# Kernel tuning notes

Measured on AMD Instinct MI355X. Metric: run time of the kernel, lower is better.

Reference implementation:

```python
import jax, jax.numpy as jnp
import numpy as np
import math

N_HEAD = 4
NORM_GROUPS = 32
EPS = 1e-5


def setup_inputs() -> dict:
    key = jax.random.key(0)
    ks = jax.random.split(key, 6)
    C = 256
    x = jax.random.normal(ks[0], (2, C, 64, 64), dtype=jnp.float32)
    gn_w = jnp.ones((C,), dtype=jnp.float32)
    gn_b = jnp.zeros((C,), dtype=jnp.float32)
    s = 1.0 / math.sqrt(C)
    wq = jax.random.normal(ks[1], (C, C), dtype=jnp.float32) * s
    wk = jax.random.normal(ks[2], (C, C), dtype=jnp.float32) * s
    wv = jax.random.normal(ks[3], (C, C), dtype=jnp.float32) * s
    wo = jax.random.normal(ks[4], (C, C), dtype=jnp.float32) * s
    bo = jnp.zeros((C,), dtype=jnp.float32)
    return {"x": x, "gn_w": gn_w, "gn_b": gn_b, "wq": wq, "wk": wk,
            "wv": wv, "wo": wo, "bo": bo}


def group_norm(x, w, b):
    bsz, c, h, wd = x.shape
    xg = x.reshape(bsz, NORM_GROUPS, c // NORM_GROUPS, h, wd)
    mu = jnp.mean(xg, axis=(2, 3, 4), keepdims=True)
    var = jnp.mean(jnp.square(xg - mu), axis=(2, 3, 4), keepdims=True)
    xn = ((xg - mu) * jax.lax.rsqrt(var + EPS)).reshape(bsz, c, h, wd)
    return xn * w[None, :, None, None] + b[None, :, None, None]


def conv1x1(x, w):
    # w: (out_ch, in_ch) applied pointwise
    return jnp.einsum('bchw,oc->bohw', x, w)


def reference(x, gn_w, gn_b, wq, wk, wv, wo, bo):
    bsz, c, h, w = x.shape
    hd = c // N_HEAD
    norm = group_norm(x, gn_w, gn_b)
    q = conv1x1(norm, wq).reshape(bsz, N_HEAD, hd, h, w)
    k = conv1x1(norm, wk).reshape(bsz, N_HEAD, hd, h, w)
    v = conv1x1(norm, wv).reshape(bsz, N_HEAD, hd, h, w)
    # scores over full spatial positions; NOTE: scaled by sqrt(channel), as in source
    scores = jnp.einsum('bnchw,bncxy->bnhwxy', q, k) / jnp.sqrt(jnp.float32(c))
    probs = jax.nn.softmax(scores.reshape(bsz, N_HEAD, h, w, h * w), axis=-1)
    probs = probs.reshape(bsz, N_HEAD, h, w, h, w)
    out = jnp.einsum('bnhwxy,bncxy->bnchw', probs, v).reshape(bsz, c, h, w)
    out = conv1x1(out, wo) + bo[None, :, None, None]
    return out + x
```

## Files before the change

### kernel.cpp

```cpp
#include <hip/hip_runtime.h>

typedef float f32x4 __attribute__((ext_vector_type(4)));
typedef float f32x16 __attribute__((ext_vector_type(16)));
typedef short bf16x8 __attribute__((ext_vector_type(8)));
typedef unsigned short u16;
typedef unsigned int u32;
typedef unsigned int u32x2 __attribute__((ext_vector_type(2)));

#define MFMA(a, b, c) __builtin_amdgcn_mfma_f32_16x16x32_bf16((a), (b), (c), 0, 0, 0)
#define MFMA32(a, b, c) __builtin_amdgcn_mfma_f32_32x32x16_bf16((a), (b), (c), 0, 0, 0)

static __device__ __forceinline__ u16 f2bf(float f) {
    union { float f; u32 u; } v; v.f = f;
    u32 r = v.u + 0x7FFFu + ((v.u >> 16) & 1u);
    return (u16)(r >> 16);
}

static __device__ __forceinline__ u32 pkbf(float a, float b) {
    u32 ua = __float_as_uint(a) + 0x8000u;
    u32 ub = __float_as_uint(b) + 0x8000u;
    return __builtin_amdgcn_perm(ub, ua, 0x07060302);
}

static __device__ __forceinline__ void gll16(const u16* g, u16* l) {
    __builtin_amdgcn_global_load_lds(
        (const __attribute__((address_space(1))) u32*)(const void*)g,
        (__attribute__((address_space(3))) u32*)(void*)l, 16, 0, 0);
}

#define BAR_VM() do { \
    asm volatile("s_waitcnt vmcnt(0)" ::: "memory"); \
    __builtin_amdgcn_s_barrier(); \
    asm volatile("" ::: "memory"); \
} while (0)

#define BAR_LGKM() do { \
    asm volatile("s_waitcnt lgkmcnt(0)" ::: "memory"); \
    __builtin_amdgcn_s_barrier(); \
} while (0)

__global__ __launch_bounds__(256) void prep_kernel(
    const float* __restrict__ wq, const float* __restrict__ wk,
    const float* __restrict__ wv, const float* __restrict__ wo,
    const float* __restrict__ x, u16* __restrict__ Wbf,
    float2* __restrict__ part) {
    int blk = blockIdx.x;
    int t = threadIdx.x;
    if (blk < 256) {
        int base = (blk * 256 + t) * 4;
        int p = base >> 16;
        int off = base & 65535;
        const float* W = (p == 0) ? wq : ((p == 1) ? wk : ((p == 2) ? wv : wo));
        float sc = (p == 0) ? 0.09014009048f : 1.0f;
        float4 v = *(const float4*)(W + off);
        uint2 pk;
        pk.x = pkbf(v.x * sc, v.y * sc);
        pk.y = pkbf(v.z * sc, v.w * sc);
        *(uint2*)(Wbf + base) = pk;
        return;
    }
    int sblk = blk - 256;
    int bg = sblk >> 2, quarter = sblk & 3;
    const float* xp = x + (size_t)bg * 32768 + quarter * 8192;

    float s = 0.f, ss = 0.f;
#pragma unroll
    for (int rep = 0; rep < 8; ++rep) {
        float4 v = *(const float4*)(xp + t * 4 + rep * 1024);
        s += v.x + v.y + v.z + v.w;
        ss += v.x * v.x + v.y * v.y + v.z * v.z + v.w * v.w;
    }
    for (int off = 1; off < 64; off <<= 1) {
        s += __shfl_xor(s, off);
        ss += __shfl_xor(ss, off);
    }
    __shared__ float red[8];
    int lane = t & 63, w = t >> 6;
    if (lane == 0) { red[w] = s; red[4 + w] = ss; }
    __syncthreads();
    if (t == 0) {
        part[sblk] = make_float2(red[0] + red[1] + red[2] + red[3],
                                 red[4] + red[5] + red[6] + red[7]);
    }
}

__global__ __launch_bounds__(256) void qkv_gemm(
    const float* __restrict__ x, const float* __restrict__ gw,
    const float* __restrict__ gb, const float2* __restrict__ part,
    const u16* __restrict__ Wbf,
    u16* __restrict__ Q, u16* __restrict__ K, u16* __restrict__ V) {
    int b = blockIdx.y & 1;
    int p = blockIdx.y >> 1;
    const u16* W = Wbf + p * 65536;
    int bx = blockIdx.x;
    int m0 = ((bx >> 3) & 1) * 128;
    int n0 = ((bx & 7) | ((bx >> 4) << 3)) * 64;

    __shared__ u16 a_s[2][128 * 40];
    __shared__ u16 b_s[2][64 * 40];
    __shared__ float wgt_s[256], bia_s[256];

    int t = threadIdx.x;
    int lane = t & 63, wave = t >> 6;
    int wm = wave & 1, wn = wave >> 1;
    int r = lane & 15, qd = lane >> 4;

    {
        int c = t;
        int g = c >> 3;
        float s = 0.f, ss = 0.f;
#pragma unroll
        for (int q = 0; q < 4; ++q) {
            float2 pp = part[(b * 32 + g) * 4 + q];
            s += pp.x; ss += pp.y;
        }
        float mu = s * (1.f / 32768.f);
        float var = ss * (1.f / 32768.f) - mu * mu;
        float rstd = rsqrtf(var + 1e-5f);
        float wg = gw[c] * rstd;
        wgt_s[c] = wg;
        bia_s[c] = gb[c] - mu * wg;
    }
    __syncthreads();

    f32x4 acc[4][2];
#pragma unroll
    for (int i = 0; i < 4; ++i)
#pragma unroll
        for (int j = 0; j < 2; ++j) acc[i][j] = (f32x4){0.f, 0.f, 0.f, 0.f};

    int srow = t >> 1;
    int scp = (t & 1) * 16;
    int bn = t & 63;
    int bw = t >> 6;
    int bswz = ((bn >> 3) & 3) ^ (((bn >> 5) & 1) << 1);
    int bgp = ((bw ^ bswz) << 3);

    uint4 pa0, pa1;
    float pxv[8];
    auto load_regs = [&](int kk) {
        const u16* src = W + (m0 + srow) * 256 + kk + scp;
        pa0 = *(const uint4*)(src);
        pa1 = *(const uint4*)(src + 8);
        const float* xcol = x + (size_t)(b * 256 + kk + bw * 8) * 4096 + n0 + bn;
#pragma unroll
        for (int j = 0; j < 8; ++j) pxv[j] = xcol[(size_t)j * 4096];
    };
    auto write_buf = [&](int bsel, int kk) {
        *(uint4*)(a_s[bsel] + srow * 40 + scp) = pa0;
        *(uint4*)(a_s[bsel] + srow * 40 + scp + 8) = pa1;
        u32* dst = (u32*)(b_s[bsel] + bn * 40 + bgp);
#pragma unroll
        for (int j = 0; j < 4; ++j) {
            int c = kk + bw * 8 + 2 * j;
            dst[j] = pkbf(pxv[2 * j] * wgt_s[c] + bia_s[c],
                          pxv[2 * j + 1] * wgt_s[c + 1] + bia_s[c + 1]);
        }
    };

    load_regs(0);
    write_buf(0, 0);
    BAR_LGKM();

    for (int it = 0; it < 8; ++it) {
        int cur = it & 1;
        bool more = (it + 1) < 8;
        if (more) load_regs((it + 1) * 32);

        bf16x8 af[4], bf[2];
#pragma unroll
        for (int mt = 0; mt < 4; ++mt)
            af[mt] = *(const bf16x8*)(a_s[cur] + (wm * 64 + mt * 16 + r) * 40 + qd * 8);
#pragma unroll
        for (int nt = 0; nt < 2; ++nt) {
            int row = wn * 32 + nt * 16 + r;
            int rswz = ((row >> 3) & 3) ^ (((row >> 5) & 1) << 1);
            bf[nt] = *(const bf16x8*)(b_s[cur] + row * 40 + ((qd ^ rswz) << 3));
        }
        if (p == 2) {
#pragma unroll
            for (int mt = 0; mt < 4; ++mt)
#pragma unroll
                for (int nt = 0; nt < 2; ++nt)
                    acc[mt][nt] = MFMA(bf[nt], af[mt], acc[mt][nt]);
        } else {
#pragma unroll
            for (int mt = 0; mt < 4; ++mt)
#pragma unroll
                for (int nt = 0; nt < 2; ++nt)
                    acc[mt][nt] = MFMA(af[mt], bf[nt], acc[mt][nt]);
        }

        if (more) write_buf(cur ^ 1, (it + 1) * 32);
        BAR_LGKM();
    }

    if (p < 2) {
        u16* dst = (p == 0) ? Q : K;
#pragma unroll
        for (int mt = 0; mt < 4; ++mt) {
#pragma unroll
            for (int nt = 0; nt < 2; ++nt) {
                int o0 = m0 + wm * 64 + mt * 16 + qd * 4;
                int s = n0 + wn * 32 + nt * 16 + r;
                int h = o0 >> 6, d0 = o0 & 63;
                uint2 pk;
                pk.x = pkbf(acc[mt][nt][0], acc[mt][nt][1]);
                pk.y = pkbf(acc[mt][nt][2], acc[mt][nt][3]);
                *(uint2*)(dst + ((size_t)((b * 4 + h) * 4096 + s)) * 64 + d0) = pk;
            }
        }
    } else {
#pragma unroll
        for (int mt = 0; mt < 4; ++mt) {
#pragma unroll
            for (int nt = 0; nt < 2; ++nt) {
                int o = m0 + wm * 64 + mt * 16 + r;
                int h = o >> 6, d = o & 63;
                int sb = n0 + wn * 32 + nt * 16 + qd * 4;
                uint2 pk;
                pk.x = pkbf(acc[mt][nt][0], acc[mt][nt][1]);
                pk.y = pkbf(acc[mt][nt][2], acc[mt][nt][3]);
                *(uint2*)(V + ((size_t)((b * 4 + h) * 64 + d)) * 4096 + sb) = pk;
            }
        }
    }
}

template <int QT>
__global__ __launch_bounds__(256, QT == 1 ? 4 : 2) void attn_kernel(
    const u16* __restrict__ Q, const u16* __restrict__ K,
    const u16* __restrict__ V, u16* __restrict__ Opart,
    float* __restrict__ Lpart, int nk32) {
    int bh = blockIdx.x & 7, sp = blockIdx.x >> 3;
    int qb = blockIdx.y;
    int t = threadIdx.x, lane = t & 63, w = t >> 6;
    int qn = lane & 31, h = lane >> 5;

    const size_t bhoff = (size_t)bh * 4096 * 64;
    int q0 = (qb * 4 + w) * (32 * QT);
    int kbase = sp * nk32 * 32;

    __shared__ u16 smem[16384];

    bf16x8 qf[QT][4];
#pragma unroll
    for (int qt = 0; qt < QT; ++qt)
#pragma unroll
        for (int c = 0; c < 4; ++c)
            qf[qt][c] = *(const bf16x8*)(Q + bhoff +
                (size_t)(q0 + qt * 32 + qn) * 64 + c * 16 + h * 8);

    f32x16 oacc[2][QT];
#pragma unroll
    for (int dt = 0; dt < 2; ++dt)
#pragma unroll
        for (int qt = 0; qt < QT; ++qt)
#pragma unroll
            for (int i = 0; i < 16; ++i) oacc[dt][qt][i] = 0.f;
    float lacc[QT];
#pragma unroll
    for (int qt = 0; qt < QT; ++qt) lacc[qt] = 0.f;

    const u16* Kp = K + bhoff;
    const u16* Vp = V + bhoff;

    int gs = (lane & 7) ^ (lane >> 3);
    int rbase = (w & 1) * 32 + (lane >> 3);

    auto fill = [&](int bufsel, int kp) {
        u16* ld = smem + bufsel * 8192 + w * 2048;
        if (w < 2) {
            const u16* s = Kp + (size_t)(kp + rbase) * 64 + gs * 8;
#pragma unroll
            for (int j = 0; j < 4; ++j) gll16(s + j * 512, ld + j * 512);
        } else {
            const u16* s = Vp + (size_t)rbase * 4096 + kp + gs * 8;
#pragma unroll
            for (int j = 0; j < 4; ++j) gll16(s + j * 32768, ld + j * 512);
        }
    };

    int sw = qn & 7;
    auto step = [&](const u16* buf, int j) {
        bf16x8 kf[4], vf[2][2];
        int kr = j * 32 + qn;
#pragma unroll
        for (int c = 0; c < 4; ++c)
            kf[c] = *(const bf16x8*)(buf + kr * 64 + (((c * 2 + h) ^ sw) << 3));
#pragma unroll
        for (int dt = 0; dt < 2; ++dt) {
            int d = dt * 32 + qn;
#pragma unroll
            for (int kc = 0; kc < 2; ++kc) {
                int g = j * 4 + kc * 2 + h;
                vf[dt][kc] = *(const bf16x8*)(buf + 4096 + d * 64 + ((g ^ sw) << 3));
            }
        }
#pragma unroll
        for (int qt = 0; qt < QT; ++qt) {
            f32x16 s;
#pragma unroll
            for (int i = 0; i < 16; ++i) s[i] = 0.f;
            __builtin_amdgcn_s_setprio(1);
#pragma unroll
            for (int c = 0; c < 4; ++c) s = MFMA32(kf[c], qf[qt][c], s);
            __builtin_amdgcn_s_setprio(0);

            float e[16];
#pragma unroll
            for (int i = 0; i < 16; ++i)
                e[i] = __builtin_amdgcn_exp2f(s[i]);
            float t0 = (e[0] + e[1]) + (e[2] + e[3]);
            float t1 = (e[4] + e[5]) + (e[6] + e[7]);
            float t2 = (e[8] + e[9]) + (e[10] + e[11]);
            float t3 = (e[12] + e[13]) + (e[14] + e[15]);
            lacc[qt] += (t0 + t1) + (t2 + t3);

            u32 p[8];
#pragma unroll
            for (int i = 0; i < 8; ++i) p[i] = pkbf(e[2 * i], e[2 * i + 1]);

            u32x2 r0 = __builtin_amdgcn_permlane32_swap(p[0], p[2], false, false);
            u32x2 r1 = __builtin_amdgcn_permlane32_swap(p[1], p[3], false, false);
            u32x2 r2 = __builtin_amdgcn_permlane32_swap(p[4], p[6], false, false);
            u32x2 r3 = __builtin_amdgcn_permlane32_swap(p[5], p[7], false, false);
            uint4 pau = {r0[0], r1[0], r0[1], r1[1]};
            uint4 pbu = {r2[0], r3[0], r2[1], r3[1]};
            bf16x8 pA = *(const bf16x8*)&pau;
            bf16x8 pB = *(const bf16x8*)&pbu;

            __builtin_amdgcn_s_setprio(1);
#pragma unroll
            for (int dt = 0; dt < 2; ++dt) {
                oacc[dt][qt] = MFMA32(vf[dt][0], pA, oacc[dt][qt]);
                oacc[dt][qt] = MFMA32(vf[dt][1], pB, oacc[dt][qt]);
            }
            __builtin_amdgcn_s_setprio(0);
        }
    };

    int npair = nk32 >> 1;
    fill(0, kbase);
    if (npair > 1) fill(1, kbase + 64);
    BAR_VM();

    for (int i = 0; i < npair; ++i) {
        const u16* cur = smem + (i & 1) * 8192;
        step(cur, 0);
        step(cur, 1);
        BAR_VM();
        if (i + 2 < npair) fill(i & 1, kbase + (i + 2) * 64);
    }

    float lfull[QT];
#pragma unroll
    for (int qt = 0; qt < QT; ++qt)
        lfull[qt] = lacc[qt] + __shfl_xor(lacc[qt], 32);

    u16* my = smem + w * (32 * 72);
    size_t obase = ((size_t)sp * 8 + bh) * 4096 + q0;
#pragma unroll
    for (int qt = 0; qt < QT; ++qt) {
#pragma unroll
        for (int dt = 0; dt < 2; ++dt) {
#pragma unroll
            for (int g = 0; g < 4; ++g) {
                int d0 = g * 8 + h * 4 + dt * 32;
                uint2 pk;
                pk.x = pkbf(oacc[dt][qt][4 * g], oacc[dt][qt][4 * g + 1]);
                pk.y = pkbf(oacc[dt][qt][4 * g + 2], oacc[dt][qt][4 * g + 3]);
                *(uint2*)(my + qn * 72 + d0) = pk;
            }
        }
#pragma unroll
        for (int rr = 0; rr < 4; ++rr) {
            int row = rr * 8 + (lane >> 3), ch = lane & 7;
            uint4 v = *(const uint4*)(my + row * 72 + ch * 8);
            *(uint4*)(Opart + (obase + qt * 32 + row) * 64 + ch * 8) = v;
        }
    }
    if (h == 0) {
#pragma unroll
        for (int qt = 0; qt < QT; ++qt)
            Lpart[obase + qt * 32 + qn] = lfull[qt];
    }
}

__global__ __launch_bounds__(256) void attn_combine(
    const u16* __restrict__ Opart, const float* __restrict__ Lpart,
    u16* __restrict__ attnT, int nsplit) {
    int t = threadIdx.x;
    int gr = blockIdx.x * 64 + (t >> 2);
    int d0 = (t & 3) * 16;

    float l = 0.f;
    for (int s = 0; s < nsplit; ++s) l += Lpart[(size_t)s * 32768 + gr];
    float inv = 1.f / l;

    float acc[16];
#pragma unroll
    for (int i = 0; i < 16; ++i) acc[i] = 0.f;
    for (int s = 0; s < nsplit; ++s) {
        const u16* p = Opart + ((size_t)s * 32768 + gr) * 64 + d0;
        uint4 a = *(const uint4*)(p);
        uint4 bq = *(const uint4*)(p + 8);
        const u32* ap = (const u32*)&a;
        const u32* bp = (const u32*)&bq;
#pragma unroll
        for (int j = 0; j < 4; ++j) {
            acc[2 * j]     += __uint_as_float(ap[j] << 16);
            acc[2 * j + 1] += __uint_as_float(ap[j] & 0xFFFF0000u);
            acc[8 + 2 * j]     += __uint_as_float(bp[j] << 16);
            acc[8 + 2 * j + 1] += __uint_as_float(bp[j] & 0xFFFF0000u);
        }
    }
    u32 pk[8];
#pragma unroll
    for (int j = 0; j < 8; ++j)
        pk[j] = pkbf(acc[2 * j] * inv, acc[2 * j + 1] * inv);

    int bh = gr >> 12, q = gr & 4095;
    int b = bh >> 2, hh = bh & 3;
    u16* dst = attnT + ((size_t)(b * 4096 + q)) * 256 + hh * 64 + d0;
    *(uint4*)(dst) = make_uint4(pk[0], pk[1], pk[2], pk[3]);
    *(uint4*)(dst + 8) = make_uint4(pk[4], pk[5], pk[6], pk[7]);
}

__global__ __launch_bounds__(256) void out_gemm(
    const u16* __restrict__ attnT, const u16* __restrict__ W3,
    const float* __restrict__ bo, const float* __restrict__ x,
    float* __restrict__ out) {
    int b = blockIdx.y;
    int bx = blockIdx.x;
    int m0 = ((bx >> 3) & 3) * 64;
    int n0 = ((bx & 7) | ((bx >> 5) << 3)) * 64;

    __shared__ u16 a_s[2][64 * 40];
    __shared__ u16 b_s[2][64 * 40];

    int t = threadIdx.x;
    int lane = t & 63, wave = t >> 6;
    int wm = wave & 1, wn = wave >> 1;
    int r = lane & 15, qd = lane >> 4;

    const u16* Bsrc = attnT + (size_t)b * 4096 * 256;

    f32x4 acc[2][2];
#pragma unroll
    for (int i = 0; i < 2; ++i)
#pragma unroll
        for (int j = 0; j < 2; ++j) acc[i][j] = (f32x4){0.f, 0.f, 0.f, 0.f};

    int u = t & 127;
    int srow = u >> 1;
    int scp = (u & 1) * 16;

    uint4 p0, p1;
    auto load_regs = [&](int kk) {
        const u16* src = (t < 128)
            ? W3 + (m0 + srow) * 256 + kk + scp
            : Bsrc + (size_t)(n0 + srow) * 256 + kk + scp;
        p0 = *(const uint4*)(src);
        p1 = *(const uint4*)(src + 8);
    };
    auto write_buf = [&](int bsel) {
        u16* dst = (t < 128) ? (a_s[bsel] + srow * 40 + scp)
                             : (b_s[bsel] + srow * 40 + scp);
        *(uint4*)(dst) = p0;
        *(uint4*)(dst + 8) = p1;
    };

    load_regs(0);
    write_buf(0);
    BAR_LGKM();

    for (int it = 0; it < 8; ++it) {
        int cur = it & 1;
        bool more = (it + 1) < 8;
        if (more) load_regs((it + 1) * 32);

        bf16x8 af[2], bf[2];
#pragma unroll
        for (int mt = 0; mt < 2; ++mt)
            af[mt] = *(const bf16x8*)(a_s[cur] + (wm * 32 + mt * 16 + r) * 40 + qd * 8);
#pragma unroll
        for (int nt = 0; nt < 2; ++nt)
            bf[nt] = *(const bf16x8*)(b_s[cur] + (wn * 32 + nt * 16 + r) * 40 + qd * 8);
#pragma unroll
        for (int mt = 0; mt < 2; ++mt)
#pragma unroll
            for (int nt = 0; nt < 2; ++nt)
                acc[mt][nt] = MFMA(af[mt], bf[nt], acc[mt][nt]);

        if (more) write_buf(cur ^ 1);
        BAR_LGKM();
    }

#pragma unroll
    for (int mt = 0; mt < 2; ++mt) {
#pragma unroll
        for (int nt = 0; nt < 2; ++nt) {
#pragma unroll
            for (int j = 0; j < 4; ++j) {
                int o = m0 + wm * 32 + mt * 16 + qd * 4 + j;
                int s = n0 + wn * 32 + nt * 16 + r;
                size_t idx = (size_t)(b * 256 + o) * 4096 + s;
                out[idx] = acc[mt][nt][j] + bo[o] + x[idx];
            }
        }
    }
}

extern "C" void kernel_launch(void* const* d_in, const int* in_sizes, int n_in,
                              void* d_out, int out_size, void* d_ws, size_t ws_size,
                              hipStream_t stream) {
    const float* x = (const float*)d_in[0];
    const float* gn_w = (const float*)d_in[1];
    const float* gn_b = (const float*)d_in[2];
    const float* wq = (const float*)d_in[3];
    const float* wk = (const float*)d_in[4];
    const float* wv = (const float*)d_in[5];
    const float* wo = (const float*)d_in[6];
    const float* bo = (const float*)d_in[7];
    float* out = (float*)d_out;

    char* ws = (char*)d_ws;
    u16* attnT = (u16*)(ws);
    u16* Q     = (u16*)(ws + (4u << 20));
    u16* Kp    = (u16*)(ws + (8u << 20));
    u16* Vp    = (u16*)(ws + (12u << 20));
    u16* Wbf   = (u16*)(ws + (16u << 20));
    float2* part = (float2*)(ws + (16u << 20) + 524288);

    size_t opart_off = (size_t)17 << 20;
    size_t osplit = 8ull * 4096 * 64 * 2;
    int nsplit = (ws_size >= opart_off + 4 * osplit + 4ull * 32768 * 4 + 4096) ? 4 : 2;
    u16* Opart = (u16*)(ws + opart_off);
    float* Lpart = (float*)(ws + opart_off + (size_t)nsplit * osplit);

    prep_kernel<<<512, 256, 0, stream>>>(wq, wk, wv, wo, x, Wbf, part);
    qkv_gemm<<<dim3(128, 6), 256, 0, stream>>>(x, gn_w, gn_b, part, Wbf, Q, Kp, Vp);
    attn_kernel<1><<<dim3(8 * nsplit, 32), 256, 0, stream>>>(
        Q, Kp, Vp, Opart, Lpart, 128 / nsplit);
    attn_combine<<<512, 256, 0, stream>>>(Opart, Lpart, attnT, nsplit);
    out_gemm<<<dim3(256, 2), 256, 0, stream>>>(attnT, Wbf + 3 * 65536, bo, x, out);
}
```

Before: 139.8 us.

## Fuse split-attention combine into output projection GEMM with full-K LDS tiles

Removes the separate attn_combine kernel and the attnT intermediate buffer. The output GEMM now reduces the split partial outputs itself, normalizes by the summed L values, and writes the bf16 tile into LDS. It then runs the full K=256 loop from LDS using an XOR-swizzled layout and a larger 128x64 tile. This saves one kernel launch and one global round trip. In exchange it uses more shared memory per block, launches half as many blocks, and gives up load/compute overlap inside the GEMM.

```diff
diff --git a/kernel.cpp b/kernel.cpp
--- a/kernel.cpp
+++ b/kernel.cpp
@@ -20,6 +20,13 @@
     u32 ua = __float_as_uint(a) + 0x8000u;
     u32 ub = __float_as_uint(b) + 0x8000u;
     return __builtin_amdgcn_perm(ub, ua, 0x07060302);
+}
+
+static __device__ __forceinline__ float bflo(u32 v) {
+    return __uint_as_float(v << 16);
+}
+static __device__ __forceinline__ float bfhi(u32 v) {
+    return __uint_as_float(v & 0xFFFF0000u);
 }
 
 static __device__ __forceinline__ void gll16(const u16* g, u16* l) {
@@ -387,123 +394,103 @@
     }
 }
 
-__global__ __launch_bounds__(256) void attn_combine(
+__global__ __launch_bounds__(256) void out_fused(
     const u16* __restrict__ Opart, const float* __restrict__ Lpart,
-    u16* __restrict__ attnT, int nsplit) {
-    int t = threadIdx.x;
-    int gr = blockIdx.x * 64 + (t >> 2);
-    int d0 = (t & 3) * 16;
-
-    float l = 0.f;
-    for (int s = 0; s < nsplit; ++s) l += Lpart[(size_t)s * 32768 + gr];
-    float inv = 1.f / l;
-
-    float acc[16];
-#pragma unroll
-    for (int i = 0; i < 16; ++i) acc[i] = 0.f;
-    for (int s = 0; s < nsplit; ++s) {
-        const u16* p = Opart + ((size_t)s * 32768 + gr) * 64 + d0;
-        uint4 a = *(const uint4*)(p);
-        uint4 bq = *(const uint4*)(p + 8);
-        const u32* ap = (const u32*)&a;
-        const u32* bp = (const u32*)&bq;
-#pragma unroll
-        for (int j = 0; j < 4; ++j) {
-            acc[2 * j]     += __uint_as_float(ap[j] << 16);
-            acc[2 * j + 1] += __uint_as_float(ap[j] & 0xFFFF0000u);
-            acc[8 + 2 * j]     += __uint_as_float(bp[j] << 16);
-            acc[8 + 2 * j + 1] += __uint_as_float(bp[j] & 0xFFFF0000u);
-        }
-    }
-    u32 pk[8];
-#pragma unroll
-    for (int j = 0; j < 8; ++j)
-        pk[j] = pkbf(acc[2 * j] * inv, acc[2 * j + 1] * inv);
-
-    int bh = gr >> 12, q = gr & 4095;
-    int b = bh >> 2, hh = bh & 3;
-    u16* dst = attnT + ((size_t)(b * 4096 + q)) * 256 + hh * 64 + d0;
-    *(uint4*)(dst) = make_uint4(pk[0], pk[1], pk[2], pk[3]);
-    *(uint4*)(dst + 8) = make_uint4(pk[4], pk[5], pk[6], pk[7]);
-}
-
-__global__ __launch_bounds__(256) void out_gemm(
-    const u16* __restrict__ attnT, const u16* __restrict__ W3,
-    const float* __restrict__ bo, const float* __restrict__ x,
-    float* __restrict__ out) {
+    const u16* __restrict__ W3, const float* __restrict__ bo,
+    const float* __restrict__ x, float* __restrict__ out, int nsplit) {
     int b = blockIdx.y;
     int bx = blockIdx.x;
-    int m0 = ((bx >> 3) & 3) * 64;
-    int n0 = ((bx & 7) | ((bx >> 5) << 3)) * 64;
-
-    __shared__ u16 a_s[2][64 * 40];
-    __shared__ u16 b_s[2][64 * 40];
+    int m0 = ((bx >> 3) & 1) * 128;
+    int n0 = ((bx & 7) | ((bx >> 4) << 3)) * 64;
+
+    __shared__ u16 a_s[128 * 264];
+    __shared__ u16 b_s[64 * 264];
+    __shared__ float linv_s[4][64];
 
     int t = threadIdx.x;
     int lane = t & 63, wave = t >> 6;
     int wm = wave & 1, wn = wave >> 1;
     int r = lane & 15, qd = lane >> 4;
 
-    const u16* Bsrc = attnT + (size_t)b * 4096 * 256;
-
-    f32x4 acc[2][2];
-#pragma unroll
-    for (int i = 0; i < 2; ++i)
+    {
+        int hh = t >> 6, row = t & 63;
+        size_t gi = (size_t)(b * 4 + hh) * 4096 + n0 + row;
+        float l = 0.f;
+        for (int s = 0; s < nsplit; ++s) l += Lpart[(size_t)s * 32768 + gi];
+        linv_s[hh][row] = 1.f / l;
+    }
+    {
+        int kg = t & 31, r0 = t >> 5;
+#pragma unroll
+        for (int j = 0; j < 16; ++j) {
+            int row = r0 + j * 8;
+            uint4 v = *(const uint4*)(W3 + (m0 + row) * 256 + kg * 8);
+            int g = kg ^ (row & 7);
+            *(uint4*)(a_s + row * 264 + g * 8) = v;
+        }
+    }
+    __syncthreads();
+
+    {
+        int dg = t & 7, r0 = (t >> 3) & 31;
+#pragma unroll
+        for (int j = 0; j < 8; ++j) {
+            int hh = j >> 1, row = r0 + (j & 1) * 32;
+            size_t base = ((size_t)(b * 4 + hh) * 4096 + n0 + row) * 64 + dg * 8;
+            float a0 = 0.f, a1 = 0.f, a2 = 0.f, a3 = 0.f;
+            float a4 = 0.f, a5 = 0.f, a6 = 0.f, a7 = 0.f;
+            for (int s = 0; s < nsplit; ++s) {
+                uint4 v = *(const uint4*)(Opart + (size_t)s * 2097152 + base);
+                a0 += bflo(v.x); a1 += bfhi(v.x);
+                a2 += bflo(v.y); a3 += bfhi(v.y);
+                a4 += bflo(v.z); a5 += bfhi(v.z);
+                a6 += bflo(v.w); a7 += bfhi(v.w);
+            }
+            float li = linv_s[hh][row];
+            int g = (hh * 8 + dg) ^ (row & 7);
+            uint4 pk;
+            pk.x = pkbf(a0 * li, a1 * li);
+            pk.y = pkbf(a2 * li, a3 * li);
+            pk.z = pkbf(a4 * li, a5 * li);
+            pk.w = pkbf(a6 * li, a7 * li);
+            *(uint4*)(b_s + row * 264 + g * 8) = pk;
+        }
+    }
+    __syncthreads();
+
+    f32x4 acc[4][2];
+#pragma unroll
+    for (int i = 0; i < 4; ++i)
 #pragma unroll
         for (int j = 0; j < 2; ++j) acc[i][j] = (f32x4){0.f, 0.f, 0.f, 0.f};
 
-    int u = t & 127;
-    int srow = u >> 1;
-    int scp = (u & 1) * 16;
-
-    uint4 p0, p1;
-    auto load_regs = [&](int kk) {
-        const u16* src = (t < 128)
-            ? W3 + (m0 + srow) * 256 + kk + scp
-            : Bsrc + (size_t)(n0 + srow) * 256 + kk + scp;
-        p0 = *(const uint4*)(src);
-        p1 = *(const uint4*)(src + 8);
-    };
-    auto write_buf = [&](int bsel) {
-        u16* dst = (t < 128) ? (a_s[bsel] + srow * 40 + scp)
-                             : (b_s[bsel] + srow * 40 + scp);
-        *(uint4*)(dst) = p0;
-        *(uint4*)(dst + 8) = p1;
-    };
-
-    load_regs(0);
-    write_buf(0);
-    BAR_LGKM();
-
-    for (int it = 0; it < 8; ++it) {
-        int cur = it & 1;
-        bool more = (it + 1) < 8;
-        if (more) load_regs((it + 1) * 32);
-
-        bf16x8 af[2], bf[2];
-#pragma unroll
-        for (int mt = 0; mt < 2; ++mt)
-            af[mt] = *(const bf16x8*)(a_s[cur] + (wm * 32 + mt * 16 + r) * 40 + qd * 8);
-#pragma unroll
-        for (int nt = 0; nt < 2; ++nt)
-            bf[nt] = *(const bf16x8*)(b_s[cur] + (wn * 32 + nt * 16 + r) * 40 + qd * 8);
-#pragma unroll
-        for (int mt = 0; mt < 2; ++mt)
+    for (int kk = 0; kk < 256; kk += 32) {
+        int kg = kk >> 3;
+        bf16x8 af[4], bf[2];
+#pragma unroll
+        for (int mt = 0; mt < 4; ++mt) {
+            int row = wm * 64 + mt * 16 + r;
+            af[mt] = *(const bf16x8*)(a_s + row * 264 + (((kg + qd) ^ (row & 7)) << 3));
+        }
+#pragma unroll
+        for (int nt = 0; nt < 2; ++nt) {
+            int row = wn * 32 + nt * 16 + r;
+            bf[nt] = *(const bf16x8*)(b_s + row * 264 + (((kg + qd) ^ (row & 7)) << 3));
+        }
+#pragma unroll
+        for (int mt = 0; mt < 4; ++mt)
 #pragma unroll
             for (int nt = 0; nt < 2; ++nt)
                 acc[mt][nt] = MFMA(af[mt], bf[nt], acc[mt][nt]);
-
-        if (more) write_buf(cur ^ 1);
-        BAR_LGKM();
-    }
-
-#pragma unroll
-    for (int mt = 0; mt < 2; ++mt) {
+    }
+
+#pragma unroll
+    for (int mt = 0; mt < 4; ++mt) {
 #pragma unroll
         for (int nt = 0; nt < 2; ++nt) {
 #pragma unroll
             for (int j = 0; j < 4; ++j) {
-                int o = m0 + wm * 32 + mt * 16 + qd * 4 + j;
+                int o = m0 + wm * 64 + mt * 16 + qd * 4 + j;
                 int s = n0 + wn * 32 + nt * 16 + r;
                 size_t idx = (size_t)(b * 256 + o) * 4096 + s;
                 out[idx] = acc[mt][nt][j] + bo[o] + x[idx];
@@ -526,7 +513,6 @@
     float* out = (float*)d_out;
 
     char* ws = (char*)d_ws;
-    u16* attnT = (u16*)(ws);
     u16* Q     = (u16*)(ws + (4u << 20));
     u16* Kp    = (u16*)(ws + (8u << 20));
     u16* Vp    = (u16*)(ws + (12u << 20));
@@ -543,6 +529,6 @@
     qkv_gemm<<<dim3(128, 6), 256, 0, stream>>>(x, gn_w, gn_b, part, Wbf, Q, Kp, Vp);
     attn_kernel<1><<<dim3(8 * nsplit, 32), 256, 0, stream>>>(
         Q, Kp, Vp, Opart, Lpart, 128 / nsplit);
-    attn_combine<<<512, 256, 0, stream>>>(Opart, Lpart, attnT, nsplit);
-    out_gemm<<<dim3(256, 2), 256, 0, stream>>>(attnT, Wbf + 3 * 65536, bo, x, out);
-}
+    out_fused<<<dim3(128, 2), 256, 0, stream>>>(
+        Opart, Lpart, Wbf + 3 * 65536, bo, x, out, nsplit);
+}
```

Result: slower. 145.6 us (+4.1%).
